# Optimization experiments

Measured on AMD Instinct MI355X. Metric: run time of the kernel, lower is better.

Reference implementation:

```python
import jax, jax.numpy as jnp
import numpy as np

LORA_ALPHA = 16.0
TOP_K = 2


def setup_inputs() -> dict:
    key = jax.random.key(0)
    k_x, k_w, k_g, k_a, k_b = jax.random.split(key, 5)
    B, S, H, O, E, R = 2, 2048, 2048, 2048, 8, 16
    x = jax.random.normal(k_x, (B, S, H), dtype=jnp.float32)
    weight = jax.random.normal(k_w, (O, H), dtype=jnp.float32)          # frozen base W [out, in]
    gate_w = jax.random.normal(k_g, (E, H), dtype=jnp.float32) * 0.02   # router gate [E, in]
    A_w = jax.random.normal(k_a, (E, R, H), dtype=jnp.float32) * (1.0 / np.sqrt(H))  # stacked lora_A
    B_w = jax.random.normal(k_b, (E, O, R), dtype=jnp.float32) * 0.01   # stacked lora_B
    return {"x": x, "weight": weight, "gate_w": gate_w, "A_w": A_w, "B_w": B_w}


def reference(x, weight, gate_w, A_w, B_w):
    E = gate_w.shape[0]
    # Base frozen linear: F.linear(x, weight)
    out = jnp.einsum("bsh,oh->bso", x, weight)

    # Router: softmax over experts, top-2, renormalize
    logits = jnp.einsum("bsh,eh->bse", x, gate_w)
    probs = jax.nn.softmax(logits, axis=-1)
    topk_w, topk_idx = jax.lax.top_k(probs, TOP_K)          # [b,s,2]
    topk_w = topk_w / jnp.sum(topk_w, axis=-1, keepdims=True)

    # Per-token combine weight for each expert (sum over the 2 slots)
    onehot = jax.nn.one_hot(topk_idx, E, dtype=x.dtype)      # [b,s,2,E]
    cw = jnp.einsum("bsk,bske->bse", topk_w, onehot)         # [b,s,E]

    # LoRA: down-project into all experts' rank spaces, weight, then up-project.
    # t: [b,s,E,r] is small (r=16); weighting here avoids a [b,s,E,out] buffer.
    t = jnp.einsum("bsh,erh->bser", x, A_w)
    t = t * cw[..., None]
    lora = jnp.einsum("bser,eor->bso", t, B_w)

    return out + LORA_ALPHA * lora
```

## Files before the change

kernel.cpp:

```cpp
#include <hip/hip_runtime.h>
#include <hip/hip_bf16.h>


typedef __bf16 bf16x8 __attribute__((ext_vector_type(8)));
typedef float f32x4 __attribute__((ext_vector_type(4)));

__device__ __forceinline__ __bf16 f2bf(float f) {
  union { float f; unsigned u; } v; v.f = f;
  unsigned r = (v.u + 0x7FFFu + ((v.u >> 16) & 1u)) >> 16;
  unsigned short s = (unsigned short)r;
  return __builtin_bit_cast(__bf16, s);
}

__device__ __forceinline__ void ld_lds16(const void* g, void* l) {
  __builtin_amdgcn_global_load_lds((__attribute__((address_space(1))) void*)g,
                                   (__attribute__((address_space(3))) void*)l,
                                   16, 0, 0);
}

__global__ void prep_kernel(const float* __restrict__ W, const float* __restrict__ Aw,
                            const float* __restrict__ Bw, __bf16* __restrict__ Bfull,
                            __bf16* __restrict__ A2) {
  const int b = blockIdx.x, tid = threadIdx.x;
  if (b < 2176) {
    const float* src = (b < 2048) ? (W + (size_t)b * 2048)
                                  : (Aw + (size_t)(b - 2048) * 2048);
    __bf16* dst = (b < 2048) ? (Bfull + (size_t)b * 2176)
                             : (A2 + (size_t)(b - 2048) * 2048);
    const int c = tid * 8;
    float4 a = *(const float4*)(src + c);
    float4 d = *(const float4*)(src + c + 4);
    bf16x8 v;
    v[0] = f2bf(a.x); v[1] = f2bf(a.y); v[2] = f2bf(a.z); v[3] = f2bf(a.w);
    v[4] = f2bf(d.x); v[5] = f2bf(d.y); v[6] = f2bf(d.z); v[7] = f2bf(d.w);
    *(bf16x8*)(dst + c) = v;
  } else {
    const int idx = (b - 2176) * 256 + tid;
    const int e = idx >> 11, o = idx & 2047;
    const float4* s = (const float4*)(Bw + ((size_t)e * 2048 + o) * 16);
    float4 v0 = s[0], v1 = s[1], v2 = s[2], v3 = s[3];
    __bf16* d = Bfull + (size_t)o * 2176 + 2048 + e * 16;
    bf16x8 lo, hi;
    lo[0] = f2bf(v0.x); lo[1] = f2bf(v0.y); lo[2] = f2bf(v0.z); lo[3] = f2bf(v0.w);
    lo[4] = f2bf(v1.x); lo[5] = f2bf(v1.y); lo[6] = f2bf(v1.z); lo[7] = f2bf(v1.w);
    hi[0] = f2bf(v2.x); hi[1] = f2bf(v2.y); hi[2] = f2bf(v2.z); hi[3] = f2bf(v2.w);
    hi[4] = f2bf(v3.x); hi[5] = f2bf(v3.y); hi[6] = f2bf(v3.z); hi[7] = f2bf(v3.w);
    *(bf16x8*)d = lo;
    *(bf16x8*)(d + 8) = hi;
  }
}

__global__ __launch_bounds__(256) void router_t2(
    const float* __restrict__ x, const float* __restrict__ gw,
    const __bf16* __restrict__ A2, __bf16* __restrict__ Abuf) {
  __shared__ __align__(16) __bf16 xs[16][2056];
  __shared__ float red[4][16][8];
  __shared__ float cws[16][8];
  const int tid = threadIdx.x;
  const int wave = tid >> 6, lane = tid & 63;
  const int t0 = blockIdx.x * 16;

#pragma unroll 4
  for (int i = 0; i < 16; ++i) {
    const float* xr = x + (size_t)(t0 + i) * 2048 + tid * 8;
    float4 a = *(const float4*)xr;
    float4 b = *(const float4*)(xr + 4);
    bf16x8 v;
    v[0] = f2bf(a.x); v[1] = f2bf(a.y); v[2] = f2bf(a.z); v[3] = f2bf(a.w);
    v[4] = f2bf(b.x); v[5] = f2bf(b.y); v[6] = f2bf(b.z); v[7] = f2bf(b.w);
    *(bf16x8*)(Abuf + (size_t)(t0 + i) * 2176 + tid * 8) = v;
    *(bf16x8*)&xs[i][tid * 8] = v;
  }
  __syncthreads();

  const int tok = tid & 15, slc = tid >> 4;
  const int c0 = slc * 128;
  float acc[8] = {0, 0, 0, 0, 0, 0, 0, 0};
  for (int j8 = 0; j8 < 16; ++j8) {
    bf16x8 xv = *(const bf16x8*)&xs[tok][c0 + j8 * 8];
    float xf[8];
#pragma unroll
    for (int j = 0; j < 8; ++j) xf[j] = (float)xv[j];
#pragma unroll
    for (int e = 0; e < 8; ++e) {
      float4 g0 = *(const float4*)(gw + e * 2048 + c0 + j8 * 8);
      float4 g1 = *(const float4*)(gw + e * 2048 + c0 + j8 * 8 + 4);
      acc[e] += xf[0] * g0.x + xf[1] * g0.y + xf[2] * g0.z + xf[3] * g0.w +
                xf[4] * g1.x + xf[5] * g1.y + xf[6] * g1.z + xf[7] * g1.w;
    }
  }
#pragma unroll
  for (int e = 0; e < 8; ++e) {
    acc[e] += __shfl_down(acc[e], 16);
    acc[e] += __shfl_down(acc[e], 32);
  }
  if (lane < 16) {
#pragma unroll
    for (int e = 0; e < 8; ++e) red[wave][lane][e] = acc[e];
  }
  __syncthreads();
  if (tid < 16) {
    float lg[8];
#pragma unroll
    for (int e = 0; e < 8; ++e)
      lg[e] = red[0][tid][e] + red[1][tid][e] + red[2][tid][e] + red[3][tid][e];
    int a = 0;
    for (int e = 1; e < 8; ++e) if (lg[e] > lg[a]) a = e;
    int b = (a == 0) ? 1 : 0;
    for (int e = 0; e < 8; ++e) if (e != a && lg[e] > lg[b]) b = e;
    const float d = __expf(lg[b] - lg[a]);
    float o[8] = {0, 0, 0, 0, 0, 0, 0, 0};
    o[a] = 1.0f / (1.0f + d);
    o[b] = d / (1.0f + d);
#pragma unroll
    for (int e = 0; e < 8; ++e) cws[tid][e] = o[e];
  }
  __syncthreads();

  const int m = lane & 15, q = lane >> 4;
  const int nt0 = wave * 2;
  f32x4 tacc[2] = {};
  for (int ks = 0; ks < 64; ++ks) {
    bf16x8 af = *(const bf16x8*)&xs[m][ks * 32 + q * 8];
#pragma unroll
    for (int h = 0; h < 2; ++h) {
      bf16x8 bfg = *(const bf16x8*)(A2 + (size_t)((nt0 + h) * 16 + m) * 2048 +
                                    ks * 32 + q * 8);
      tacc[h] = __builtin_amdgcn_mfma_f32_16x16x32_bf16(af, bfg, tacc[h], 0, 0, 0);
    }
  }
#pragma unroll
  for (int h = 0; h < 2; ++h) {
    const int nt = nt0 + h;
#pragma unroll
    for (int rg = 0; rg < 4; ++rg) {
      const int trow = q * 4 + rg;
      const float s = tacc[h][rg] * 16.0f * cws[trow][nt];
      Abuf[(size_t)(t0 + trow) * 2176 + 2048 + nt * 16 + m] = f2bf(s);
    }
  }
}

__global__ __launch_bounds__(512, 2) void mfma_gemm_bt2(
    const __bf16* __restrict__ A, const __bf16* __restrict__ B,
    float* __restrict__ C, int lda, int ldb, int ldc, int kiters) {
  __shared__ __align__(16) __bf16 lds[3 * 24576];
  const int tid = threadIdx.x;
  const int wave = tid >> 6;
  const int lane = tid & 63;

  const int wg = blockIdx.x + (blockIdx.y << 4);
  const int swz = (wg & 7) * 32 + (wg >> 3);
  const int tm = (swz & 15) * 256;
  const int tn = (swz >> 4) * 128;

  const int srow = lane >> 3;
  const int skoff = ((lane & 7) ^ srow) * 8;

  const int wr = wave >> 1, wc = wave & 1;
  const int rlo = lane & 7;
  const int rb3 = (lane >> 3) & 1;
  const int qb = lane >> 4;

  f32x4 acc[4][4] = {};

  auto stage = [&](int buf, int kt) {
    const int kc = kt * 64;
    __bf16* Ls = lds + buf * 24576;
#pragma unroll
    for (int r = 0; r < 4; ++r) {
      const int ch = wave + r * 8;
      ld_lds16(A + (size_t)(tm + ch * 8 + srow) * lda + kc + skoff, &Ls[ch * 512]);
    }
#pragma unroll
    for (int r = 0; r < 2; ++r) {
      const int ch = wave + r * 8;
      ld_lds16(B + (size_t)(tn + ch * 8 + srow) * ldb + kc + skoff,
               &Ls[16384 + ch * 512]);
    }
  };

  stage(0, 0);
  stage(1, 1);
  asm volatile("s_waitcnt vmcnt(6)" ::: "memory");
  __builtin_amdgcn_s_barrier();

  int cb = 0;
  for (int kt = 0; kt < kiters; ++kt) {
    const bool pf = (kt + 2 < kiters);
    if (pf) stage((kt + 2) % 3, kt + 2);

    const __bf16* As = lds + cb * 24576;
    const __bf16* Bs = As + 16384;
#pragma unroll
    for (int ks = 0; ks < 2; ++ks) {
      bf16x8 af[4], bfg[4];
      const int q8 = ((ks * 4 + qb) ^ rlo) * 8;
#pragma unroll
      for (int i = 0; i < 4; ++i) {
        const int rh = wr * 8 + i * 2 + rb3;
        af[i] = *(const bf16x8*)&As[rh * 512 + rlo * 64 + q8];
      }
#pragma unroll
      for (int j = 0; j < 4; ++j) {
        const int rh = wc * 8 + j * 2 + rb3;
        bfg[j] = *(const bf16x8*)&Bs[rh * 512 + rlo * 64 + q8];
      }
      __builtin_amdgcn_s_setprio(1);
#pragma unroll
      for (int i = 0; i < 4; ++i)
#pragma unroll
        for (int j = 0; j < 4; ++j)
          acc[i][j] =
              __builtin_amdgcn_mfma_f32_16x16x32_bf16(af[i], bfg[j], acc[i][j], 0, 0, 0);
      __builtin_amdgcn_s_setprio(0);
    }
    asm volatile("s_waitcnt lgkmcnt(0)" ::: "memory");
    if (pf) {
      asm volatile("s_waitcnt vmcnt(6)" ::: "memory");
    } else {
      asm volatile("s_waitcnt vmcnt(0)" ::: "memory");
    }
    __builtin_amdgcn_s_barrier();
    cb = (cb + 1 == 3) ? 0 : cb + 1;
  }

  const int crow0 = tm + wr * 64 + (lane >> 4) * 4;
  const int ccol0 = tn + wc * 64 + (lane & 15);
#pragma unroll
  for (int i = 0; i < 4; ++i)
#pragma unroll
    for (int j = 0; j < 4; ++j)
#pragma unroll
      for (int rg = 0; rg < 4; ++rg)
        C[(size_t)(crow0 + i * 16 + rg) * ldc + ccol0 + j * 16] = acc[i][j][rg];
}

extern "C" void kernel_launch(void* const* d_in, const int* in_sizes, int n_in,
                              void* d_out, int out_size, void* d_ws, size_t ws_size,
                              hipStream_t stream) {
  const float* x = (const float*)d_in[0];
  const float* weight = (const float*)d_in[1];
  const float* gate_w = (const float*)d_in[2];
  const float* A_w = (const float*)d_in[3];
  const float* B_w = (const float*)d_in[4];
  float* out = (float*)d_out;

  char* ws = (char*)d_ws;
  __bf16* Abuf = (__bf16*)ws;
  __bf16* Bfull = (__bf16*)(ws + 17825792);
  __bf16* A2 = (__bf16*)(ws + 26738688);

  prep_kernel<<<2240, 256, 0, stream>>>(weight, A_w, B_w, Bfull, A2);
  router_t2<<<256, 256, 0, stream>>>(x, gate_w, A2, Abuf);
  mfma_gemm_bt2<<<dim3(16, 16), 512, 0, stream>>>(Abuf, Bfull, out, 2176, 2176,
                                                  2048, 34);
}
```

Before: 164.7 us.

## Split-K across wave halves with interleaved staging and XCD-aware tile mapping

The GEMM now gives each group of four waves its own half of every 64-wide K slice. Each wave computes a 128x64 sub-tile, loaded as two A halves interleaved with split global-to-LDS prefetches and extra barriers. The two K-half partial sums are reduced through LDS before the store. The block-to-tile mapping is changed so each XCD covers a contiguous 4x8 region of tiles, to improve L2 locality. The aim is to raise MFMA work per LDS read and overlap loads with compute, at the cost of twice the accumulator registers (occupancy risk under the 512x2 launch bounds), more barriers, and an LDS reduction epilogue.

```diff
diff --git a/kernel.cpp b/kernel.cpp
--- a/kernel.cpp
+++ b/kernel.cpp
@@ -141,7 +141,7 @@
   }
 }
 
-__global__ __launch_bounds__(512, 2) void mfma_gemm_bt2(
+__global__ __launch_bounds__(512, 2) void mfma_gemm_bt3(
     const __bf16* __restrict__ A, const __bf16* __restrict__ B,
     float* __restrict__ C, int lda, int ldb, int ldc, int kiters) {
   __shared__ __align__(16) __bf16 lds[3 * 24576];
@@ -150,90 +150,130 @@
   const int lane = tid & 63;
 
   const int wg = blockIdx.x + (blockIdx.y << 4);
-  const int swz = (wg & 7) * 32 + (wg >> 3);
-  const int tm = (swz & 15) * 256;
-  const int tn = (swz >> 4) * 128;
+  const int xcd = wg & 7, loc = wg >> 3;
+  const int tm = ((xcd & 3) * 4 + (loc & 3)) * 256;
+  const int tn = ((xcd >> 2) * 8 + (loc >> 2)) * 128;
 
   const int srow = lane >> 3;
   const int skoff = ((lane & 7) ^ srow) * 8;
 
-  const int wr = wave >> 1, wc = wave & 1;
+  const int wid = wave & 3;
+  const int wr = wid >> 1, wc = wid & 1;
+  const int ks4 = (wave >> 2) * 4;
   const int rlo = lane & 7;
   const int rb3 = (lane >> 3) & 1;
   const int qb = lane >> 4;
-
-  f32x4 acc[4][4] = {};
-
-  auto stage = [&](int buf, int kt) {
+  const int q8 = ((ks4 + qb) ^ rlo) * 8;
+
+  f32x4 acc[8][4] = {};
+
+  auto stageA = [&](int buf, int kt) {
     const int kc = kt * 64;
     __bf16* Ls = lds + buf * 24576;
 #pragma unroll
-    for (int r = 0; r < 4; ++r) {
+    for (int r = 0; r < 3; ++r) {
       const int ch = wave + r * 8;
       ld_lds16(A + (size_t)(tm + ch * 8 + srow) * lda + kc + skoff, &Ls[ch * 512]);
     }
+  };
+  auto stageB = [&](int buf, int kt) {
+    const int kc = kt * 64;
+    __bf16* Ls = lds + buf * 24576;
+    const int ch = wave + 24;
+    ld_lds16(A + (size_t)(tm + ch * 8 + srow) * lda + kc + skoff, &Ls[ch * 512]);
 #pragma unroll
     for (int r = 0; r < 2; ++r) {
-      const int ch = wave + r * 8;
-      ld_lds16(B + (size_t)(tn + ch * 8 + srow) * ldb + kc + skoff,
-               &Ls[16384 + ch * 512]);
+      const int bh = wave + r * 8;
+      ld_lds16(B + (size_t)(tn + bh * 8 + srow) * ldb + kc + skoff,
+               &Ls[16384 + bh * 512]);
     }
   };
 
-  stage(0, 0);
-  stage(1, 1);
+  stageA(0, 0); stageB(0, 0);
+  stageA(1, 1); stageB(1, 1);
   asm volatile("s_waitcnt vmcnt(6)" ::: "memory");
   __builtin_amdgcn_s_barrier();
 
   int cb = 0;
   for (int kt = 0; kt < kiters; ++kt) {
     const bool pf = (kt + 2 < kiters);
-    if (pf) stage((kt + 2) % 3, kt + 2);
-
+    const int nb = (kt + 2) % 3;
     const __bf16* As = lds + cb * 24576;
     const __bf16* Bs = As + 16384;
-#pragma unroll
-    for (int ks = 0; ks < 2; ++ks) {
-      bf16x8 af[4], bfg[4];
-      const int q8 = ((ks * 4 + qb) ^ rlo) * 8;
-#pragma unroll
-      for (int i = 0; i < 4; ++i) {
-        const int rh = wr * 8 + i * 2 + rb3;
-        af[i] = *(const bf16x8*)&As[rh * 512 + rlo * 64 + q8];
-      }
-#pragma unroll
-      for (int j = 0; j < 4; ++j) {
-        const int rh = wc * 8 + j * 2 + rb3;
-        bfg[j] = *(const bf16x8*)&Bs[rh * 512 + rlo * 64 + q8];
-      }
-      __builtin_amdgcn_s_setprio(1);
-#pragma unroll
-      for (int i = 0; i < 4; ++i)
-#pragma unroll
-        for (int j = 0; j < 4; ++j)
-          acc[i][j] =
-              __builtin_amdgcn_mfma_f32_16x16x32_bf16(af[i], bfg[j], acc[i][j], 0, 0, 0);
-      __builtin_amdgcn_s_setprio(0);
-    }
+
+    bf16x8 af[4], bfg[4];
+#pragma unroll
+    for (int j = 0; j < 4; ++j) {
+      const int rh = wc * 8 + j * 2 + rb3;
+      bfg[j] = *(const bf16x8*)&Bs[rh * 512 + rlo * 64 + q8];
+    }
+#pragma unroll
+    for (int i = 0; i < 4; ++i) {
+      const int rh = wr * 16 + i * 2 + rb3;
+      af[i] = *(const bf16x8*)&As[rh * 512 + rlo * 64 + q8];
+    }
+    if (pf) stageA(nb, kt + 2);
+    __builtin_amdgcn_s_barrier();
     asm volatile("s_waitcnt lgkmcnt(0)" ::: "memory");
+    __builtin_amdgcn_s_setprio(1);
+#pragma unroll
+    for (int i = 0; i < 4; ++i)
+#pragma unroll
+      for (int j = 0; j < 4; ++j)
+        acc[i][j] =
+            __builtin_amdgcn_mfma_f32_16x16x32_bf16(af[i], bfg[j], acc[i][j], 0, 0, 0);
+    __builtin_amdgcn_s_setprio(0);
+    __builtin_amdgcn_s_barrier();
+
+    bf16x8 ag[4];
+#pragma unroll
+    for (int i = 0; i < 4; ++i) {
+      const int rh = wr * 16 + 8 + i * 2 + rb3;
+      ag[i] = *(const bf16x8*)&As[rh * 512 + rlo * 64 + q8];
+    }
     if (pf) {
+      stageB(nb, kt + 2);
       asm volatile("s_waitcnt vmcnt(6)" ::: "memory");
     } else {
       asm volatile("s_waitcnt vmcnt(0)" ::: "memory");
     }
     __builtin_amdgcn_s_barrier();
+    asm volatile("s_waitcnt lgkmcnt(0)" ::: "memory");
+    __builtin_amdgcn_s_setprio(1);
+#pragma unroll
+    for (int i = 0; i < 4; ++i)
+#pragma unroll
+      for (int j = 0; j < 4; ++j)
+        acc[4 + i][j] =
+            __builtin_amdgcn_mfma_f32_16x16x32_bf16(ag[i], bfg[j], acc[4 + i][j], 0, 0, 0);
+    __builtin_amdgcn_s_setprio(0);
+    __builtin_amdgcn_s_barrier();
     cb = (cb + 1 == 3) ? 0 : cb + 1;
   }
 
-  const int crow0 = tm + wr * 64 + (lane >> 4) * 4;
-  const int ccol0 = tn + wc * 64 + (lane & 15);
-#pragma unroll
-  for (int i = 0; i < 4; ++i)
-#pragma unroll
-    for (int j = 0; j < 4; ++j)
-#pragma unroll
-      for (int rg = 0; rg < 4; ++rg)
-        C[(size_t)(crow0 + i * 16 + rg) * ldc + ccol0 + j * 16] = acc[i][j][rg];
+  float* red = (float*)lds;
+  if (wave >= 4) {
+#pragma unroll
+    for (int i = 0; i < 8; ++i)
+#pragma unroll
+      for (int j = 0; j < 4; ++j)
+        *(f32x4*)&red[(i * 4 + j) * 1024 + wid * 256 + lane * 4] = acc[i][j];
+  }
+  __syncthreads();
+  if (wave < 4) {
+    const int crow0 = tm + wr * 128 + (lane >> 4) * 4;
+    const int ccol0 = tn + wc * 64 + (lane & 15);
+#pragma unroll
+    for (int i = 0; i < 8; ++i)
+#pragma unroll
+      for (int j = 0; j < 4; ++j) {
+        f32x4 v = acc[i][j] +
+                  *(const f32x4*)&red[(i * 4 + j) * 1024 + wid * 256 + lane * 4];
+#pragma unroll
+        for (int rg = 0; rg < 4; ++rg)
+          C[(size_t)(crow0 + i * 16 + rg) * ldc + ccol0 + j * 16] = v[rg];
+      }
+  }
 }
 
 extern "C" void kernel_launch(void* const* d_in, const int* in_sizes, int n_in,
@@ -253,6 +293,6 @@
 
   prep_kernel<<<2240, 256, 0, stream>>>(weight, A_w, B_w, Bfull, A2);
   router_t2<<<256, 256, 0, stream>>>(x, gate_w, A2, Abuf);
-  mfma_gemm_bt2<<<dim3(16, 16), 512, 0, stream>>>(Abuf, Bfull, out, 2176, 2176,
+  mfma_gemm_bt3<<<dim3(16, 16), 512, 0, stream>>>(Abuf, Bfull, out, 2176, 2176,
                                                   2048, 34);
 }
```

Result: no change. 162.7 us (-1.2%).
